# Performance work log

Hardware: AMD Instinct MI355X
Metric: run time of the kernel (lower is better)

The kernel has to match this reference:

```python
import jax, jax.numpy as jnp
import numpy as np

B, N_ELEC, N_NUC, D_EMB, D_MSG = 512, 32, 8, 128, 128


def idx_perm(n):
    # ordered pairs (i, j), i != j, shaped [n, n-1]
    i = np.repeat(np.arange(n), n - 1).reshape(n, n - 1)
    j = np.array([[k for k in range(n) if k != ii] for ii in range(n)])
    return jnp.asarray(i), jnp.asarray(j)


def pairwise_diffs(a, b):
    # a: [..., n, 3], b: [..., m, 3] -> [..., n, m, 4] (dx, dy, dz, |d|^2)
    d = a[..., :, None, :] - b[..., None, :, :]
    return jnp.concatenate([d, jnp.sum(d * d, axis=-1, keepdims=True)], axis=-1)


def mlp(x, w1, b1, w2, b2):
    return jax.nn.silu(x @ w1 + b1) @ w2 + b2


def setup_inputs() -> dict:
    key = jax.random.key(0)
    ks = jax.random.split(key, 10)
    sc = 0.1
    return {
        'rs': jax.random.normal(ks[0], (B, N_ELEC, 3), jnp.float32),
        'coords': jax.random.normal(ks[1], (N_NUC, 3), jnp.float32),
        'messages_el': jax.random.normal(ks[2], (B, N_ELEC, N_ELEC - 1, D_MSG), jnp.float32),
        'messages_nuc': jax.random.normal(ks[3], (B, N_ELEC, N_NUC, D_MSG), jnp.float32),
        'emb': jax.random.normal(ks[4], (B, N_ELEC, D_EMB), jnp.float32),
        'w1_el': jax.random.normal(ks[5], (D_EMB + D_MSG, 256), jnp.float32) * sc,
        'b1_el': jnp.zeros((256,), jnp.float32),
        'w2_el': jax.random.normal(ks[6], (256, 1), jnp.float32) * sc,
        'b2_el': jnp.zeros((1,), jnp.float32),
        'w1_nuc': jax.random.normal(ks[7], (D_EMB + D_MSG, 256), jnp.float32) * sc,
        'b1_nuc': jnp.zeros((256,), jnp.float32),
        'w2_nuc': jax.random.normal(ks[8], (256, 1), jnp.float32) * sc,
        'b2_nuc': jnp.zeros((1,), jnp.float32),
        'nuc_charges': jnp.array([6.0, 1.0, 1.0, 1.0, 1.0, 1.0, 1.0, 1.0], jnp.float32),
    }


def reference(rs, coords, messages_el, messages_nuc, emb,
              w1_el, b1_el, w2_el, b2_el,
              w1_nuc, b1_nuc, w2_nuc, b2_nuc, nuc_charges):
    n_elec, n_nuc = rs.shape[-2], coords.shape[0]
    emb_p = emb[:, :, None]  # [B, n_elec, 1, D_emb]
    # gather-concat features per pair
    f_el = jnp.concatenate(
        [jnp.broadcast_to(emb_p, (B, n_elec, n_elec - 1, D_EMB)), messages_el], axis=-1)
    f_nuc = jnp.concatenate(
        [jnp.broadcast_to(emb_p, (B, n_elec, n_nuc, D_EMB)), messages_nuc], axis=-1)
    i, j = idx_perm(n_elec)
    diffs_nuc = pairwise_diffs(rs, coords)  # [B, n_elec, n_nuc, 4]
    diffs_ee = pairwise_diffs(-rs, -rs)[:, i, j]  # [B, n_elec, n_elec-1, 4]
    diffs = jnp.concatenate([diffs_ee, diffs_nuc], axis=-2)
    f = jnp.concatenate(
        [mlp(f_el, w1_el, b1_el, w2_el, b2_el),
         mlp(f_nuc, w1_nuc, b1_nuc, w2_nuc, b2_nuc)], axis=-2)  # [B, n_elec, P, 1]
    ps = f * diffs[..., :3] / (1.0 + diffs[..., 3:] ** 1.5)
    ps = ps.sum(axis=-2)  # [B, n_elec, 3]
    # deeperwin decay
    decay = jnp.tanh(diffs_nuc[..., -1] / (0.5 / nuc_charges) ** 2).prod(axis=-1)
    return np.exp(-3.5).astype(np.float32) * decay[..., None] * ps
```

## Files before the change

kernel.cpp:

```cpp
#include <hip/hip_runtime.h>
#include <hip/hip_bf16.h>

#define OUT_SCALE 0.030197383422318501f

typedef __attribute__((ext_vector_type(8))) short bf16x8;
typedef __attribute__((ext_vector_type(4))) float f32x4;

#define EL_BLOCKS 1024
#define NUC_BLOCKS 1024

__device__ __forceinline__ unsigned pk2(float a, float b) {
  __hip_bfloat162 h = __float22bfloat162_rn(make_float2(a, b));
  unsigned u;
  __builtin_memcpy(&u, &h, 4);
  return u;
}

__device__ __forceinline__ float silu_f(float h) {
  return h * __builtin_amdgcn_rcpf(1.0f + __expf(-h));
}

__global__ void prep_w1(const float* __restrict__ w1a,
                        const float* __restrict__ w1b,
                        unsigned short* __restrict__ wp) {
  int gid = blockIdx.x * 256 + threadIdx.x;
  const float* w1 = (gid < 8192) ? w1a : w1b;
  int rem = gid & 8191;
  int kk = rem >> 10;
  int kg = (rem >> 8) & 3;
  int col = rem & 255;
  const float* src = w1 + (kk * 32 + kg * 8) * 256 + col;
  uint4 v;
  v.x = pk2(src[0 * 256], src[1 * 256]);
  v.y = pk2(src[2 * 256], src[3 * 256]);
  v.z = pk2(src[4 * 256], src[5 * 256]);
  v.w = pk2(src[6 * 256], src[7 * 256]);
  *(uint4*)(wp + (size_t)gid * 8) = v;
}

__global__ __launch_bounds__(512, 4) void bf_main_kernel(
    const float* __restrict__ rs, const float* __restrict__ msg_el,
    const float* __restrict__ msg_nuc, const float* __restrict__ emb,
    const unsigned short* __restrict__ wpk,
    const float* __restrict__ b1_el, const float* __restrict__ w2_el,
    const float* __restrict__ b2_el,
    const float* __restrict__ b1_nuc, const float* __restrict__ w2_nuc,
    const float* __restrict__ b2_nuc,
    const float* __restrict__ coords, const float* __restrict__ chg,
    float* __restrict__ out) {
  __shared__ __align__(16) unsigned short s_emb[16 * 128];
  __shared__ __align__(16) unsigned short s_msg[2 * 64 * 128];
  __shared__ __align__(16) float s_embc[16 * 256];
  __shared__ float s_fp[8][512];
  __shared__ float s_ps[16][4];
  __shared__ float s_decay[16];

  const int tid = threadIdx.x;
  const int bid = blockIdx.x;
  const int lane = tid & 63;
  const int wv = tid >> 6;
  const int cIdx = lane & 15, kg = lane >> 4;

  if (bid < EL_BLOCKS) {
    const int gp0 = bid * 16;
    const float* msg = msg_el;

    if (tid < 64) ((float*)s_ps)[tid] = 0.0f;

    if (tid < 256) {
      int p = tid >> 4, ch = tid & 15;
      const float* src = emb + (gp0 + p) * 128 + ch * 8;
      float4 v0 = *(const float4*)src;
      float4 v1 = *(const float4*)(src + 4);
      uint4 pk;
      pk.x = pk2(v0.x, v0.y); pk.y = pk2(v0.z, v0.w);
      pk.z = pk2(v1.x, v1.y); pk.w = pk2(v1.z, v1.w);
      *(uint4*)(s_emb + p * 128 + (ch ^ p) * 8) = pk;
    }

    bf16x8 Bf[4][2];
    float b1v[2][4], w2v[2][4];
    const int col = wv * 32 + cIdx;
#pragma unroll
    for (int nt = 0; nt < 2; ++nt) {
#pragma unroll
      for (int reg = 0; reg < 4; ++reg) {
        int h = wv * 32 + nt * 16 + kg * 4 + reg;
        b1v[nt][reg] = b1_el[h];
        w2v[nt][reg] = w2_el[h];
      }
#pragma unroll
      for (int kk = 0; kk < 4; ++kk)
        Bf[kk][nt] = *(const bf16x8*)(
            wpk + (size_t)((kk * 4 + kg) * 256 + col + nt * 16) * 8);
    }

    float4 la[2], lb[2];
#pragma unroll
    for (int u = 0; u < 2; ++u) {
      int id = u * 512 + tid;
      int lrw = id >> 4, ch = id & 15;
      int p = lrw >> 5, j = lrw & 31;
      int jc = j < 31 ? j : 30;
      const float* s = msg + (size_t)((gp0 + p) * 31 + jc) * 128 + ch * 8;
      la[u] = *(const float4*)s;
      lb[u] = *(const float4*)(s + 4);
    }

    __syncthreads();

    {
      f32x4 aE0 = {b1v[0][0], b1v[0][1], b1v[0][2], b1v[0][3]};
      f32x4 aE1 = {b1v[1][0], b1v[1][1], b1v[1][2], b1v[1][3]};
#pragma unroll
      for (int kk = 0; kk < 4; ++kk) {
        bf16x8 a = *(const bf16x8*)(
            s_emb + cIdx * 128 + ((kk * 4 + kg) ^ cIdx) * 8);
        aE0 = __builtin_amdgcn_mfma_f32_16x16x32_bf16(Bf[kk][0], a, aE0, 0, 0, 0);
        aE1 = __builtin_amdgcn_mfma_f32_16x16x32_bf16(Bf[kk][1], a, aE1, 0, 0, 0);
      }
      *(f32x4*)(s_embc + cIdx * 256 + wv * 32 + kg * 4) = aE0;
      *(f32x4*)(s_embc + cIdx * 256 + wv * 32 + 16 + kg * 4) = aE1;
    }

#pragma unroll
    for (int nt = 0; nt < 2; ++nt)
#pragma unroll
      for (int kk = 0; kk < 4; ++kk)
        Bf[kk][nt] = *(const bf16x8*)(
            wpk + (size_t)(((kk + 4) * 4 + kg) * 256 + col + nt * 16) * 8);

#pragma unroll
    for (int u = 0; u < 2; ++u) {
      int id = u * 512 + tid;
      int lrw = id >> 4, ch = id & 15;
      uint4 pk;
      pk.x = pk2(la[u].x, la[u].y); pk.y = pk2(la[u].z, la[u].w);
      pk.z = pk2(lb[u].x, lb[u].y); pk.w = pk2(lb[u].z, lb[u].w);
      *(uint4*)(s_msg + lrw * 128 + ((ch ^ (lrw & 15)) * 8)) = pk;
    }

    __syncthreads();

#pragma unroll 1
    for (int c = 0; c < 8; ++c) {
      if (c < 7) {
#pragma unroll
        for (int u = 0; u < 2; ++u) {
          int id = u * 512 + tid;
          int lrw = id >> 4, ch = id & 15;
          int p = ((c + 1) << 1) + (lrw >> 5);
          int j = lrw & 31;
          int jc = j < 31 ? j : 30;
          const float* s = msg + (size_t)((gp0 + p) * 31 + jc) * 128 + ch * 8;
          la[u] = *(const float4*)s;
          lb[u] = *(const float4*)(s + 4);
        }
      }
      const unsigned short* mb = s_msg + (c & 1) * 8192;
#pragma unroll
      for (int tt = 0; tt < 4; ++tt) {
        int p = (c << 1) + (tt >> 1);
        const float* ec = s_embc + p * 256;
        f32x4 acc0 = *(const f32x4*)(ec + wv * 32 + kg * 4);
        f32x4 acc1 = *(const f32x4*)(ec + wv * 32 + 16 + kg * 4);
        const unsigned short* mp = mb + (tt * 16 + cIdx) * 128;
#pragma unroll
        for (int kk = 0; kk < 4; ++kk) {
          bf16x8 a = *(const bf16x8*)(mp + ((kk * 4 + kg) ^ cIdx) * 8);
          acc0 = __builtin_amdgcn_mfma_f32_16x16x32_bf16(Bf[kk][0], a, acc0, 0, 0, 0);
          acc1 = __builtin_amdgcn_mfma_f32_16x16x32_bf16(Bf[kk][1], a, acc1, 0, 0, 0);
        }
        float p0 = 0.0f, p1 = 0.0f;
#pragma unroll
        for (int reg = 0; reg < 4; ++reg) {
          p0 += silu_f(acc0[reg]) * w2v[0][reg];
          p1 += silu_f(acc1[reg]) * w2v[1][reg];
        }
        float v = p0 + p1;
        v += __shfl_xor(v, 16);
        v += __shfl_xor(v, 32);
        if (kg == 0) s_fp[wv][c * 64 + tt * 16 + cIdx] = v;
      }
      if (c < 7) {
#pragma unroll
        for (int u = 0; u < 2; ++u) {
          int id = u * 512 + tid;
          int lrw = id >> 4, ch = id & 15;
          uint4 pk;
          pk.x = pk2(la[u].x, la[u].y); pk.y = pk2(la[u].z, la[u].w);
          pk.z = pk2(lb[u].x, lb[u].y); pk.w = pk2(lb[u].z, lb[u].w);
          *(uint4*)(s_msg + ((c + 1) & 1) * 8192 + lrw * 128 +
                    ((ch ^ (lrw & 15)) * 8)) = pk;
        }
      }
      __syncthreads();
    }

    if (tid < 496) {
      int p = tid / 31, jj = tid - p * 31;
      int gp = gp0 + p, b = gp >> 5, i = gp & 31;
      int jidx = jj + (jj >= i ? 1 : 0);
      const float* rsb = rs + b * 96;
      float dx = rsb[jidx * 3 + 0] - rsb[i * 3 + 0];
      float dy = rsb[jidx * 3 + 1] - rsb[i * 3 + 1];
      float dz = rsb[jidx * 3 + 2] - rsb[i * 3 + 2];
      float tq = dx * dx + dy * dy + dz * dz;
      int row = p * 32 + jj;
      float f = b2_el[0];
#pragma unroll
      for (int w = 0; w < 8; ++w) f += s_fp[w][row];
      float g = f * __builtin_amdgcn_rcpf(1.0f + tq * sqrtf(tq));
      atomicAdd(&s_ps[p][0], g * dx);
      atomicAdd(&s_ps[p][1], g * dy);
      atomicAdd(&s_ps[p][2], g * dz);
    }
    if (tid < 16) {
      int gp = gp0 + tid, b = gp >> 5, i = gp & 31;
      float x = rs[(b * 32 + i) * 3 + 0];
      float y = rs[(b * 32 + i) * 3 + 1];
      float z = rs[(b * 32 + i) * 3 + 2];
      float dcy = 1.0f;
#pragma unroll
      for (int n = 0; n < 8; ++n) {
        float dx = x - coords[n * 3 + 0];
        float dy = y - coords[n * 3 + 1];
        float dz = z - coords[n * 3 + 2];
        float tq = dx * dx + dy * dy + dz * dz;
        float zc = chg[n];
        dcy *= tanhf(4.0f * tq * zc * zc);
      }
      s_decay[tid] = dcy;
    }
    __syncthreads();
    if (tid < 48) {
      int p = tid / 3, c = tid - p * 3;
      int gp = gp0 + p;
      atomicAdd(&out[gp * 3 + c], OUT_SCALE * s_decay[p] * s_ps[p][c]);
    }
  } else {
    const int nbid = bid - EL_BLOCKS;
    const int gp0 = nbid * 16;
    const float* msg = msg_nuc;
    const unsigned short* wp = wpk + 8192 * 8;

    if (tid < 64) ((float*)s_ps)[tid] = 0.0f;

    if (tid < 256) {
      int p = tid >> 4, ch = tid & 15;
      const float* src = emb + (gp0 + p) * 128 + ch * 8;
      float4 v0 = *(const float4*)src;
      float4 v1 = *(const float4*)(src + 4);
      uint4 pk;
      pk.x = pk2(v0.x, v0.y); pk.y = pk2(v0.z, v0.w);
      pk.z = pk2(v1.x, v1.y); pk.w = pk2(v1.z, v1.w);
      *(uint4*)(s_emb + p * 128 + (ch ^ p) * 8) = pk;
    }

    bf16x8 Bf[4][2];
    float b1v[2][4], w2v[2][4];
    const int col = wv * 32 + cIdx;
#pragma unroll
    for (int nt = 0; nt < 2; ++nt) {
#pragma unroll
      for (int reg = 0; reg < 4; ++reg) {
        int h = wv * 32 + nt * 16 + kg * 4 + reg;
        b1v[nt][reg] = b1_nuc[h];
        w2v[nt][reg] = w2_nuc[h];
      }
#pragma unroll
      for (int kk = 0; kk < 4; ++kk)
        Bf[kk][nt] = *(const bf16x8*)(
            wp + (size_t)((kk * 4 + kg) * 256 + col + nt * 16) * 8);
    }

    float4 la[2], lb[2];
#pragma unroll
    for (int u = 0; u < 2; ++u) {
      int id = u * 512 + tid;
      int lrw = id >> 4, ch = id & 15;
      const float* s = msg + (size_t)(gp0 * 8 + lrw) * 128 + ch * 8;
      la[u] = *(const float4*)s;
      lb[u] = *(const float4*)(s + 4);
    }

    __syncthreads();

    {
      f32x4 aE0 = {b1v[0][0], b1v[0][1], b1v[0][2], b1v[0][3]};
      f32x4 aE1 = {b1v[1][0], b1v[1][1], b1v[1][2], b1v[1][3]};
#pragma unroll
      for (int kk = 0; kk < 4; ++kk) {
        bf16x8 a = *(const bf16x8*)(
            s_emb + cIdx * 128 + ((kk * 4 + kg) ^ cIdx) * 8);
        aE0 = __builtin_amdgcn_mfma_f32_16x16x32_bf16(Bf[kk][0], a, aE0, 0, 0, 0);
        aE1 = __builtin_amdgcn_mfma_f32_16x16x32_bf16(Bf[kk][1], a, aE1, 0, 0, 0);
      }
      *(f32x4*)(s_embc + cIdx * 256 + wv * 32 + kg * 4) = aE0;
      *(f32x4*)(s_embc + cIdx * 256 + wv * 32 + 16 + kg * 4) = aE1;
    }

#pragma unroll
    for (int nt = 0; nt < 2; ++nt)
#pragma unroll
      for (int kk = 0; kk < 4; ++kk)
        Bf[kk][nt] = *(const bf16x8*)(
            wp + (size_t)(((kk + 4) * 4 + kg) * 256 + col + nt * 16) * 8);

#pragma unroll
    for (int u = 0; u < 2; ++u) {
      int id = u * 512 + tid;
      int lrw = id >> 4, ch = id & 15;
      uint4 pk;
      pk.x = pk2(la[u].x, la[u].y); pk.y = pk2(la[u].z, la[u].w);
      pk.z = pk2(lb[u].x, lb[u].y); pk.w = pk2(lb[u].z, lb[u].w);
      *(uint4*)(s_msg + lrw * 128 + ((ch ^ (lrw & 15)) * 8)) = pk;
    }

    __syncthreads();

#pragma unroll 1
    for (int c = 0; c < 2; ++c) {
      if (c < 1) {
#pragma unroll
        for (int u = 0; u < 2; ++u) {
          int id = u * 512 + tid;
          int lrw = id >> 4, ch = id & 15;
          const float* s = msg + (size_t)(gp0 * 8 + 64 + lrw) * 128 + ch * 8;
          la[u] = *(const float4*)s;
          lb[u] = *(const float4*)(s + 4);
        }
      }
      const unsigned short* mb = s_msg + (c & 1) * 8192;
#pragma unroll
      for (int tt = 0; tt < 4; ++tt) {
        int t = c * 4 + tt;
        int r = t * 16 + cIdx;
        int p = r >> 3;
        const float* ec = s_embc + p * 256;
        f32x4 acc0 = *(const f32x4*)(ec + wv * 32 + kg * 4);
        f32x4 acc1 = *(const f32x4*)(ec + wv * 32 + 16 + kg * 4);
        const unsigned short* mp = mb + (r & 63) * 128;
#pragma unroll
        for (int kk = 0; kk < 4; ++kk) {
          bf16x8 a = *(const bf16x8*)(mp + ((kk * 4 + kg) ^ cIdx) * 8);
          acc0 = __builtin_amdgcn_mfma_f32_16x16x32_bf16(Bf[kk][0], a, acc0, 0, 0, 0);
          acc1 = __builtin_amdgcn_mfma_f32_16x16x32_bf16(Bf[kk][1], a, acc1, 0, 0, 0);
        }
        float p0 = 0.0f, p1 = 0.0f;
#pragma unroll
        for (int reg = 0; reg < 4; ++reg) {
          p0 += silu_f(acc0[reg]) * w2v[0][reg];
          p1 += silu_f(acc1[reg]) * w2v[1][reg];
        }
        float v = p0 + p1;
        v += __shfl_xor(v, 16);
        v += __shfl_xor(v, 32);
        if (kg == 0) s_fp[wv][t * 16 + cIdx] = v;
      }
      if (c < 1) {
#pragma unroll
        for (int u = 0; u < 2; ++u) {
          int id = u * 512 + tid;
          int lrw = id >> 4, ch = id & 15;
          uint4 pk;
          pk.x = pk2(la[u].x, la[u].y); pk.y = pk2(la[u].z, la[u].w);
          pk.z = pk2(lb[u].x, lb[u].y); pk.w = pk2(lb[u].z, lb[u].w);
          *(uint4*)(s_msg + 8192 + lrw * 128 + ((ch ^ (lrw & 15)) * 8)) = pk;
        }
      }
      __syncthreads();
    }

    if (tid < 128) {
      int p = tid >> 3, n = tid & 7;
      int gp = gp0 + p, b = gp >> 5, i = gp & 31;
      float dx = rs[(b * 32 + i) * 3 + 0] - coords[n * 3 + 0];
      float dy = rs[(b * 32 + i) * 3 + 1] - coords[n * 3 + 1];
      float dz = rs[(b * 32 + i) * 3 + 2] - coords[n * 3 + 2];
      float tq = dx * dx + dy * dy + dz * dz;
      float f = b2_nuc[0];
#pragma unroll
      for (int w = 0; w < 8; ++w) f += s_fp[w][tid];
      float g = f * __builtin_amdgcn_rcpf(1.0f + tq * sqrtf(tq));
      atomicAdd(&s_ps[p][0], g * dx);
      atomicAdd(&s_ps[p][1], g * dy);
      atomicAdd(&s_ps[p][2], g * dz);
    }
    if (tid < 16) {
      int gp = gp0 + tid, b = gp >> 5, i = gp & 31;
      float x = rs[(b * 32 + i) * 3 + 0];
      float y = rs[(b * 32 + i) * 3 + 1];
      float z = rs[(b * 32 + i) * 3 + 2];
      float dcy = 1.0f;
#pragma unroll
      for (int n = 0; n < 8; ++n) {
        float dx = x - coords[n * 3 + 0];
        float dy = y - coords[n * 3 + 1];
        float dz = z - coords[n * 3 + 2];
        float tq = dx * dx + dy * dy + dz * dz;
        float zc = chg[n];
        dcy *= tanhf(4.0f * tq * zc * zc);
      }
      s_decay[tid] = dcy;
    }
    __syncthreads();
    if (tid < 48) {
      int p = tid / 3, c = tid - p * 3;
      int gp = gp0 + p;
      atomicAdd(&out[gp * 3 + c], OUT_SCALE * s_decay[p] * s_ps[p][c]);
    }
  }
}

extern "C" void kernel_launch(void* const* d_in, const int* in_sizes, int n_in,
                              void* d_out, int out_size, void* d_ws, size_t ws_size,
                              hipStream_t stream) {
  const float* rs       = (const float*)d_in[0];
  const float* coords   = (const float*)d_in[1];
  const float* msg_el   = (const float*)d_in[2];
  const float* msg_nuc  = (const float*)d_in[3];
  const float* emb      = (const float*)d_in[4];
  const float* w1_el    = (const float*)d_in[5];
  const float* b1_el    = (const float*)d_in[6];
  const float* w2_el    = (const float*)d_in[7];
  const float* b2_el    = (const float*)d_in[8];
  const float* w1_nuc   = (const float*)d_in[9];
  const float* b1_nuc   = (const float*)d_in[10];
  const float* w2_nuc   = (const float*)d_in[11];
  const float* b2_nuc   = (const float*)d_in[12];
  const float* chg      = (const float*)d_in[13];
  float* out = (float*)d_out;

  unsigned short* wpk = (unsigned short*)d_ws;

  hipMemsetAsync(out, 0, (size_t)out_size * sizeof(float), stream);
  prep_w1<<<64, 256, 0, stream>>>(w1_el, w1_nuc, wpk);
  bf_main_kernel<<<EL_BLOCKS + NUC_BLOCKS, 512, 0, stream>>>(
      rs, msg_el, msg_nuc, emb, wpk, b1_el, w2_el, b2_el, b1_nuc, w2_nuc,
      b2_nuc, coords, chg, out);
}
```

Measured before the change: 114.8 us.

## Merge electron and nucleus blocks so each block handles both MLPs and writes output directly

Each block now runs the electron-pair MLP and then the nucleus-pair MLP for the same 16 electrons, instead of splitting them across separate blocks. This halves the grid, computes decay and output once per electron, and replaces global atomics plus the output memset with plain stores. The cost is a longer serial chain per block, less parallelism across blocks, and a slightly larger shared-memory footprint.

```diff
diff --git a/kernel.cpp b/kernel.cpp
--- a/kernel.cpp
+++ b/kernel.cpp
@@ -6,8 +6,7 @@
 typedef __attribute__((ext_vector_type(8))) short bf16x8;
 typedef __attribute__((ext_vector_type(4))) float f32x4;
 
-#define EL_BLOCKS 1024
-#define NUC_BLOCKS 1024
+#define NBLOCKS 1024
 
 __device__ __forceinline__ unsigned pk2(float a, float b) {
   __hip_bfloat162 h = __float22bfloat162_rn(make_float2(a, b));
@@ -51,7 +50,8 @@
   __shared__ __align__(16) unsigned short s_emb[16 * 128];
   __shared__ __align__(16) unsigned short s_msg[2 * 64 * 128];
   __shared__ __align__(16) float s_embc[16 * 256];
-  __shared__ float s_fp[8][512];
+  __shared__ float s_fpe[8][512];
+  __shared__ float s_fpn[8][128];
   __shared__ float s_ps[16][4];
   __shared__ float s_decay[16];
 
@@ -60,356 +60,305 @@
   const int lane = tid & 63;
   const int wv = tid >> 6;
   const int cIdx = lane & 15, kg = lane >> 4;
-
-  if (bid < EL_BLOCKS) {
-    const int gp0 = bid * 16;
-    const float* msg = msg_el;
-
-    if (tid < 64) ((float*)s_ps)[tid] = 0.0f;
-
-    if (tid < 256) {
-      int p = tid >> 4, ch = tid & 15;
-      const float* src = emb + (gp0 + p) * 128 + ch * 8;
-      float4 v0 = *(const float4*)src;
-      float4 v1 = *(const float4*)(src + 4);
-      uint4 pk;
-      pk.x = pk2(v0.x, v0.y); pk.y = pk2(v0.z, v0.w);
-      pk.z = pk2(v1.x, v1.y); pk.w = pk2(v1.z, v1.w);
-      *(uint4*)(s_emb + p * 128 + (ch ^ p) * 8) = pk;
-    }
-
-    bf16x8 Bf[4][2];
-    float b1v[2][4], w2v[2][4];
-    const int col = wv * 32 + cIdx;
-#pragma unroll
-    for (int nt = 0; nt < 2; ++nt) {
+  const int gp0 = bid * 16;
+  const int col = wv * 32 + cIdx;
+
+  if (tid < 64) ((float*)s_ps)[tid] = 0.0f;
+
+  if (tid < 256) {
+    int p = tid >> 4, ch = tid & 15;
+    const float* src = emb + (gp0 + p) * 128 + ch * 8;
+    float4 v0 = *(const float4*)src;
+    float4 v1 = *(const float4*)(src + 4);
+    uint4 pk;
+    pk.x = pk2(v0.x, v0.y); pk.y = pk2(v0.z, v0.w);
+    pk.z = pk2(v1.x, v1.y); pk.w = pk2(v1.z, v1.w);
+    *(uint4*)(s_emb + p * 128 + (ch ^ p) * 8) = pk;
+  }
+
+  bf16x8 Bf[4][2];
+  float b1v[2][4], w2v[2][4];
+#pragma unroll
+  for (int nt = 0; nt < 2; ++nt) {
+#pragma unroll
+    for (int reg = 0; reg < 4; ++reg) {
+      int h = wv * 32 + nt * 16 + kg * 4 + reg;
+      b1v[nt][reg] = b1_el[h];
+      w2v[nt][reg] = w2_el[h];
+    }
+#pragma unroll
+    for (int kk = 0; kk < 4; ++kk)
+      Bf[kk][nt] = *(const bf16x8*)(
+          wpk + (size_t)((kk * 4 + kg) * 256 + col + nt * 16) * 8);
+  }
+
+  float4 la[2], lb[2];
+#pragma unroll
+  for (int u = 0; u < 2; ++u) {
+    int id = u * 512 + tid;
+    int lrw = id >> 4, ch = id & 15;
+    int p = lrw >> 5, j = lrw & 31;
+    int jc = j < 31 ? j : 30;
+    const float* s = msg_el + (size_t)((gp0 + p) * 31 + jc) * 128 + ch * 8;
+    la[u] = *(const float4*)s;
+    lb[u] = *(const float4*)(s + 4);
+  }
+
+  __syncthreads();
+
+  {
+    f32x4 aE0 = {b1v[0][0], b1v[0][1], b1v[0][2], b1v[0][3]};
+    f32x4 aE1 = {b1v[1][0], b1v[1][1], b1v[1][2], b1v[1][3]};
+#pragma unroll
+    for (int kk = 0; kk < 4; ++kk) {
+      bf16x8 a = *(const bf16x8*)(
+          s_emb + cIdx * 128 + ((kk * 4 + kg) ^ cIdx) * 8);
+      aE0 = __builtin_amdgcn_mfma_f32_16x16x32_bf16(Bf[kk][0], a, aE0, 0, 0, 0);
+      aE1 = __builtin_amdgcn_mfma_f32_16x16x32_bf16(Bf[kk][1], a, aE1, 0, 0, 0);
+    }
+    *(f32x4*)(s_embc + cIdx * 256 + wv * 32 + kg * 4) = aE0;
+    *(f32x4*)(s_embc + cIdx * 256 + wv * 32 + 16 + kg * 4) = aE1;
+  }
+
+#pragma unroll
+  for (int nt = 0; nt < 2; ++nt)
+#pragma unroll
+    for (int kk = 0; kk < 4; ++kk)
+      Bf[kk][nt] = *(const bf16x8*)(
+          wpk + (size_t)(((kk + 4) * 4 + kg) * 256 + col + nt * 16) * 8);
+
+#pragma unroll
+  for (int u = 0; u < 2; ++u) {
+    int id = u * 512 + tid;
+    int lrw = id >> 4, ch = id & 15;
+    uint4 pk;
+    pk.x = pk2(la[u].x, la[u].y); pk.y = pk2(la[u].z, la[u].w);
+    pk.z = pk2(lb[u].x, lb[u].y); pk.w = pk2(lb[u].z, lb[u].w);
+    *(uint4*)(s_msg + lrw * 128 + ((ch ^ (lrw & 15)) * 8)) = pk;
+  }
+
+  __syncthreads();
+
+#pragma unroll 1
+  for (int c = 0; c < 8; ++c) {
+    if (c < 7) {
+#pragma unroll
+      for (int u = 0; u < 2; ++u) {
+        int id = u * 512 + tid;
+        int lrw = id >> 4, ch = id & 15;
+        int p = ((c + 1) << 1) + (lrw >> 5);
+        int j = lrw & 31;
+        int jc = j < 31 ? j : 30;
+        const float* s = msg_el + (size_t)((gp0 + p) * 31 + jc) * 128 + ch * 8;
+        la[u] = *(const float4*)s;
+        lb[u] = *(const float4*)(s + 4);
+      }
+    }
+    const unsigned short* mb = s_msg + (c & 1) * 8192;
+#pragma unroll
+    for (int tt = 0; tt < 4; ++tt) {
+      int p = (c << 1) + (tt >> 1);
+      const float* ec = s_embc + p * 256;
+      f32x4 acc0 = *(const f32x4*)(ec + wv * 32 + kg * 4);
+      f32x4 acc1 = *(const f32x4*)(ec + wv * 32 + 16 + kg * 4);
+      const unsigned short* mp = mb + (tt * 16 + cIdx) * 128;
+#pragma unroll
+      for (int kk = 0; kk < 4; ++kk) {
+        bf16x8 a = *(const bf16x8*)(mp + ((kk * 4 + kg) ^ cIdx) * 8);
+        acc0 = __builtin_amdgcn_mfma_f32_16x16x32_bf16(Bf[kk][0], a, acc0, 0, 0, 0);
+        acc1 = __builtin_amdgcn_mfma_f32_16x16x32_bf16(Bf[kk][1], a, acc1, 0, 0, 0);
+      }
+      float p0 = 0.0f, p1 = 0.0f;
 #pragma unroll
       for (int reg = 0; reg < 4; ++reg) {
-        int h = wv * 32 + nt * 16 + kg * 4 + reg;
-        b1v[nt][reg] = b1_el[h];
-        w2v[nt][reg] = w2_el[h];
-      }
-#pragma unroll
-      for (int kk = 0; kk < 4; ++kk)
-        Bf[kk][nt] = *(const bf16x8*)(
-            wpk + (size_t)((kk * 4 + kg) * 256 + col + nt * 16) * 8);
-    }
-
-    float4 la[2], lb[2];
-#pragma unroll
-    for (int u = 0; u < 2; ++u) {
-      int id = u * 512 + tid;
-      int lrw = id >> 4, ch = id & 15;
-      int p = lrw >> 5, j = lrw & 31;
-      int jc = j < 31 ? j : 30;
-      const float* s = msg + (size_t)((gp0 + p) * 31 + jc) * 128 + ch * 8;
-      la[u] = *(const float4*)s;
-      lb[u] = *(const float4*)(s + 4);
-    }
-
+        p0 += silu_f(acc0[reg]) * w2v[0][reg];
+        p1 += silu_f(acc1[reg]) * w2v[1][reg];
+      }
+      float v = p0 + p1;
+      v += __shfl_xor(v, 16);
+      v += __shfl_xor(v, 32);
+      if (kg == 0) s_fpe[wv][c * 64 + tt * 16 + cIdx] = v;
+    }
+    if (c < 7) {
+#pragma unroll
+      for (int u = 0; u < 2; ++u) {
+        int id = u * 512 + tid;
+        int lrw = id >> 4, ch = id & 15;
+        uint4 pk;
+        pk.x = pk2(la[u].x, la[u].y); pk.y = pk2(la[u].z, la[u].w);
+        pk.z = pk2(lb[u].x, lb[u].y); pk.w = pk2(lb[u].z, lb[u].w);
+        *(uint4*)(s_msg + ((c + 1) & 1) * 8192 + lrw * 128 +
+                  ((ch ^ (lrw & 15)) * 8)) = pk;
+      }
+    }
     __syncthreads();
-
-    {
-      f32x4 aE0 = {b1v[0][0], b1v[0][1], b1v[0][2], b1v[0][3]};
-      f32x4 aE1 = {b1v[1][0], b1v[1][1], b1v[1][2], b1v[1][3]};
+  }
+
+  const unsigned short* wpn = wpk + 8192 * 8;
+#pragma unroll
+  for (int nt = 0; nt < 2; ++nt) {
+#pragma unroll
+    for (int reg = 0; reg < 4; ++reg) {
+      int h = wv * 32 + nt * 16 + kg * 4 + reg;
+      b1v[nt][reg] = b1_nuc[h];
+      w2v[nt][reg] = w2_nuc[h];
+    }
+#pragma unroll
+    for (int kk = 0; kk < 4; ++kk)
+      Bf[kk][nt] = *(const bf16x8*)(
+          wpn + (size_t)((kk * 4 + kg) * 256 + col + nt * 16) * 8);
+  }
+
+#pragma unroll
+  for (int u = 0; u < 2; ++u) {
+    int id = u * 512 + tid;
+    int lrw = id >> 4, ch = id & 15;
+    const float* s = msg_nuc + (size_t)(gp0 * 8 + lrw) * 128 + ch * 8;
+    la[u] = *(const float4*)s;
+    lb[u] = *(const float4*)(s + 4);
+  }
+
+  {
+    f32x4 aE0 = {b1v[0][0], b1v[0][1], b1v[0][2], b1v[0][3]};
+    f32x4 aE1 = {b1v[1][0], b1v[1][1], b1v[1][2], b1v[1][3]};
+#pragma unroll
+    for (int kk = 0; kk < 4; ++kk) {
+      bf16x8 a = *(const bf16x8*)(
+          s_emb + cIdx * 128 + ((kk * 4 + kg) ^ cIdx) * 8);
+      aE0 = __builtin_amdgcn_mfma_f32_16x16x32_bf16(Bf[kk][0], a, aE0, 0, 0, 0);
+      aE1 = __builtin_amdgcn_mfma_f32_16x16x32_bf16(Bf[kk][1], a, aE1, 0, 0, 0);
+    }
+    *(f32x4*)(s_embc + cIdx * 256 + wv * 32 + kg * 4) = aE0;
+    *(f32x4*)(s_embc + cIdx * 256 + wv * 32 + 16 + kg * 4) = aE1;
+  }
+
+#pragma unroll
+  for (int nt = 0; nt < 2; ++nt)
+#pragma unroll
+    for (int kk = 0; kk < 4; ++kk)
+      Bf[kk][nt] = *(const bf16x8*)(
+          wpn + (size_t)(((kk + 4) * 4 + kg) * 256 + col + nt * 16) * 8);
+
+#pragma unroll
+  for (int u = 0; u < 2; ++u) {
+    int id = u * 512 + tid;
+    int lrw = id >> 4, ch = id & 15;
+    uint4 pk;
+    pk.x = pk2(la[u].x, la[u].y); pk.y = pk2(la[u].z, la[u].w);
+    pk.z = pk2(lb[u].x, lb[u].y); pk.w = pk2(lb[u].z, lb[u].w);
+    *(uint4*)(s_msg + lrw * 128 + ((ch ^ (lrw & 15)) * 8)) = pk;
+  }
+
+  __syncthreads();
+
+#pragma unroll 1
+  for (int c = 0; c < 2; ++c) {
+    if (c < 1) {
+#pragma unroll
+      for (int u = 0; u < 2; ++u) {
+        int id = u * 512 + tid;
+        int lrw = id >> 4, ch = id & 15;
+        const float* s = msg_nuc + (size_t)(gp0 * 8 + 64 + lrw) * 128 + ch * 8;
+        la[u] = *(const float4*)s;
+        lb[u] = *(const float4*)(s + 4);
+      }
+    }
+    const unsigned short* mb = s_msg + (c & 1) * 8192;
+#pragma unroll
+    for (int tt = 0; tt < 4; ++tt) {
+      int t = c * 4 + tt;
+      int r = t * 16 + cIdx;
+      int p = r >> 3;
+      const float* ec = s_embc + p * 256;
+      f32x4 acc0 = *(const f32x4*)(ec + wv * 32 + kg * 4);
+      f32x4 acc1 = *(const f32x4*)(ec + wv * 32 + 16 + kg * 4);
+      const unsigned short* mp = mb + (r & 63) * 128;
 #pragma unroll
       for (int kk = 0; kk < 4; ++kk) {
-        bf16x8 a = *(const bf16x8*)(
-            s_emb + cIdx * 128 + ((kk * 4 + kg) ^ cIdx) * 8);
-        aE0 = __builtin_amdgcn_mfma_f32_16x16x32_bf16(Bf[kk][0], a, aE0, 0, 0, 0);
-        aE1 = __builtin_amdgcn_mfma_f32_16x16x32_bf16(Bf[kk][1], a, aE1, 0, 0, 0);
-      }
-      *(f32x4*)(s_embc + cIdx * 256 + wv * 32 + kg * 4) = aE0;
-      *(f32x4*)(s_embc + cIdx * 256 + wv * 32 + 16 + kg * 4) = aE1;
-    }
-
-#pragma unroll
-    for (int nt = 0; nt < 2; ++nt)
-#pragma unroll
-      for (int kk = 0; kk < 4; ++kk)
-        Bf[kk][nt] = *(const bf16x8*)(
-            wpk + (size_t)(((kk + 4) * 4 + kg) * 256 + col + nt * 16) * 8);
-
-#pragma unroll
-    for (int u = 0; u < 2; ++u) {
-      int id = u * 512 + tid;
-      int lrw = id >> 4, ch = id & 15;
-      uint4 pk;
-      pk.x = pk2(la[u].x, la[u].y); pk.y = pk2(la[u].z, la[u].w);
-      pk.z = pk2(lb[u].x, lb[u].y); pk.w = pk2(lb[u].z, lb[u].w);
-      *(uint4*)(s_msg + lrw * 128 + ((ch ^ (lrw & 15)) * 8)) = pk;
-    }
-
+        bf16x8 a = *(const bf16x8*)(mp + ((kk * 4 + kg) ^ cIdx) * 8);
+        acc0 = __builtin_amdgcn_mfma_f32_16x16x32_bf16(Bf[kk][0], a, acc0, 0, 0, 0);
+        acc1 = __builtin_amdgcn_mfma_f32_16x16x32_bf16(Bf[kk][1], a, acc1, 0, 0, 0);
+      }
+      float p0 = 0.0f, p1 = 0.0f;
+#pragma unroll
+      for (int reg = 0; reg < 4; ++reg) {
+        p0 += silu_f(acc0[reg]) * w2v[0][reg];
+        p1 += silu_f(acc1[reg]) * w2v[1][reg];
+      }
+      float v = p0 + p1;
+      v += __shfl_xor(v, 16);
+      v += __shfl_xor(v, 32);
+      if (kg == 0) s_fpn[wv][t * 16 + cIdx] = v;
+    }
+    if (c < 1) {
+#pragma unroll
+      for (int u = 0; u < 2; ++u) {
+        int id = u * 512 + tid;
+        int lrw = id >> 4, ch = id & 15;
+        uint4 pk;
+        pk.x = pk2(la[u].x, la[u].y); pk.y = pk2(la[u].z, la[u].w);
+        pk.z = pk2(lb[u].x, lb[u].y); pk.w = pk2(lb[u].z, lb[u].w);
+        *(uint4*)(s_msg + 8192 + lrw * 128 + ((ch ^ (lrw & 15)) * 8)) = pk;
+      }
+    }
     __syncthreads();
-
-#pragma unroll 1
-    for (int c = 0; c < 8; ++c) {
-      if (c < 7) {
-#pragma unroll
-        for (int u = 0; u < 2; ++u) {
-          int id = u * 512 + tid;
-          int lrw = id >> 4, ch = id & 15;
-          int p = ((c + 1) << 1) + (lrw >> 5);
-          int j = lrw & 31;
-          int jc = j < 31 ? j : 30;
-          const float* s = msg + (size_t)((gp0 + p) * 31 + jc) * 128 + ch * 8;
-          la[u] = *(const float4*)s;
-          lb[u] = *(const float4*)(s + 4);
-        }
-      }
-      const unsigned short* mb = s_msg + (c & 1) * 8192;
-#pragma unroll
-      for (int tt = 0; tt < 4; ++tt) {
-        int p = (c << 1) + (tt >> 1);
-        const float* ec = s_embc + p * 256;
-        f32x4 acc0 = *(const f32x4*)(ec + wv * 32 + kg * 4);
-        f32x4 acc1 = *(const f32x4*)(ec + wv * 32 + 16 + kg * 4);
-        const unsigned short* mp = mb + (tt * 16 + cIdx) * 128;
-#pragma unroll
-        for (int kk = 0; kk < 4; ++kk) {
-          bf16x8 a = *(const bf16x8*)(mp + ((kk * 4 + kg) ^ cIdx) * 8);
-          acc0 = __builtin_amdgcn_mfma_f32_16x16x32_bf16(Bf[kk][0], a, acc0, 0, 0, 0);
-          acc1 = __builtin_amdgcn_mfma_f32_16x16x32_bf16(Bf[kk][1], a, acc1, 0, 0, 0);
-        }
-        float p0 = 0.0f, p1 = 0.0f;
-#pragma unroll
-        for (int reg = 0; reg < 4; ++reg) {
-          p0 += silu_f(acc0[reg]) * w2v[0][reg];
-          p1 += silu_f(acc1[reg]) * w2v[1][reg];
-        }
-        float v = p0 + p1;
-        v += __shfl_xor(v, 16);
-        v += __shfl_xor(v, 32);
-        if (kg == 0) s_fp[wv][c * 64 + tt * 16 + cIdx] = v;
-      }
-      if (c < 7) {
-#pragma unroll
-        for (int u = 0; u < 2; ++u) {
-          int id = u * 512 + tid;
-          int lrw = id >> 4, ch = id & 15;
-          uint4 pk;
-          pk.x = pk2(la[u].x, la[u].y); pk.y = pk2(la[u].z, la[u].w);
-          pk.z = pk2(lb[u].x, lb[u].y); pk.w = pk2(lb[u].z, lb[u].w);
-          *(uint4*)(s_msg + ((c + 1) & 1) * 8192 + lrw * 128 +
-                    ((ch ^ (lrw & 15)) * 8)) = pk;
-        }
-      }
-      __syncthreads();
-    }
-
-    if (tid < 496) {
-      int p = tid / 31, jj = tid - p * 31;
-      int gp = gp0 + p, b = gp >> 5, i = gp & 31;
-      int jidx = jj + (jj >= i ? 1 : 0);
-      const float* rsb = rs + b * 96;
-      float dx = rsb[jidx * 3 + 0] - rsb[i * 3 + 0];
-      float dy = rsb[jidx * 3 + 1] - rsb[i * 3 + 1];
-      float dz = rsb[jidx * 3 + 2] - rsb[i * 3 + 2];
+  }
+
+  if (tid < 496) {
+    int p = tid / 31, jj = tid - p * 31;
+    int gp = gp0 + p, b = gp >> 5, i = gp & 31;
+    int jidx = jj + (jj >= i ? 1 : 0);
+    const float* rsb = rs + b * 96;
+    float dx = rsb[jidx * 3 + 0] - rsb[i * 3 + 0];
+    float dy = rsb[jidx * 3 + 1] - rsb[i * 3 + 1];
+    float dz = rsb[jidx * 3 + 2] - rsb[i * 3 + 2];
+    float tq = dx * dx + dy * dy + dz * dz;
+    int row = p * 32 + jj;
+    float f = b2_el[0];
+#pragma unroll
+    for (int w = 0; w < 8; ++w) f += s_fpe[w][row];
+    float g = f * __builtin_amdgcn_rcpf(1.0f + tq * sqrtf(tq));
+    atomicAdd(&s_ps[p][0], g * dx);
+    atomicAdd(&s_ps[p][1], g * dy);
+    atomicAdd(&s_ps[p][2], g * dz);
+  }
+  if (tid < 128) {
+    int p = tid >> 3, n = tid & 7;
+    int gp = gp0 + p, b = gp >> 5, i = gp & 31;
+    float dx = rs[(b * 32 + i) * 3 + 0] - coords[n * 3 + 0];
+    float dy = rs[(b * 32 + i) * 3 + 1] - coords[n * 3 + 1];
+    float dz = rs[(b * 32 + i) * 3 + 2] - coords[n * 3 + 2];
+    float tq = dx * dx + dy * dy + dz * dz;
+    float f = b2_nuc[0];
+#pragma unroll
+    for (int w = 0; w < 8; ++w) f += s_fpn[w][tid];
+    float g = f * __builtin_amdgcn_rcpf(1.0f + tq * sqrtf(tq));
+    atomicAdd(&s_ps[p][0], g * dx);
+    atomicAdd(&s_ps[p][1], g * dy);
+    atomicAdd(&s_ps[p][2], g * dz);
+  }
+  if (tid < 16) {
+    int gp = gp0 + tid, b = gp >> 5, i = gp & 31;
+    float x = rs[(b * 32 + i) * 3 + 0];
+    float y = rs[(b * 32 + i) * 3 + 1];
+    float z = rs[(b * 32 + i) * 3 + 2];
+    float dcy = 1.0f;
+#pragma unroll
+    for (int n = 0; n < 8; ++n) {
+      float dx = x - coords[n * 3 + 0];
+      float dy = y - coords[n * 3 + 1];
+      float dz = z - coords[n * 3 + 2];
       float tq = dx * dx + dy * dy + dz * dz;
-      int row = p * 32 + jj;
-      float f = b2_el[0];
-#pragma unroll
-      for (int w = 0; w < 8; ++w) f += s_fp[w][row];
-      float g = f * __builtin_amdgcn_rcpf(1.0f + tq * sqrtf(tq));
-      atomicAdd(&s_ps[p][0], g * dx);
-      atomicAdd(&s_ps[p][1], g * dy);
-      atomicAdd(&s_ps[p][2], g * dz);
-    }
-    if (tid < 16) {
-      int gp = gp0 + tid, b = gp >> 5, i = gp & 31;
-      float x = rs[(b * 32 + i) * 3 + 0];
-      float y = rs[(b * 32 + i) * 3 + 1];
-      float z = rs[(b * 32 + i) * 3 + 2];
-      float dcy = 1.0f;
-#pragma unroll
-      for (int n = 0; n < 8; ++n) {
-        float dx = x - coords[n * 3 + 0];
-        float dy = y - coords[n * 3 + 1];
-        float dz = z - coords[n * 3 + 2];
-        float tq = dx * dx + dy * dy + dz * dz;
-        float zc = chg[n];
-        dcy *= tanhf(4.0f * tq * zc * zc);
-      }
-      s_decay[tid] = dcy;
-    }
-    __syncthreads();
-    if (tid < 48) {
-      int p = tid / 3, c = tid - p * 3;
-      int gp = gp0 + p;
-      atomicAdd(&out[gp * 3 + c], OUT_SCALE * s_decay[p] * s_ps[p][c]);
-    }
-  } else {
-    const int nbid = bid - EL_BLOCKS;
-    const int gp0 = nbid * 16;
-    const float* msg = msg_nuc;
-    const unsigned short* wp = wpk + 8192 * 8;
-
-    if (tid < 64) ((float*)s_ps)[tid] = 0.0f;
-
-    if (tid < 256) {
-      int p = tid >> 4, ch = tid & 15;
-      const float* src = emb + (gp0 + p) * 128 + ch * 8;
-      float4 v0 = *(const float4*)src;
-      float4 v1 = *(const float4*)(src + 4);
-      uint4 pk;
-      pk.x = pk2(v0.x, v0.y); pk.y = pk2(v0.z, v0.w);
-      pk.z = pk2(v1.x, v1.y); pk.w = pk2(v1.z, v1.w);
-      *(uint4*)(s_emb + p * 128 + (ch ^ p) * 8) = pk;
-    }
-
-    bf16x8 Bf[4][2];
-    float b1v[2][4], w2v[2][4];
-    const int col = wv * 32 + cIdx;
-#pragma unroll
-    for (int nt = 0; nt < 2; ++nt) {
-#pragma unroll
-      for (int reg = 0; reg < 4; ++reg) {
-        int h = wv * 32 + nt * 16 + kg * 4 + reg;
-        b1v[nt][reg] = b1_nuc[h];
-        w2v[nt][reg] = w2_nuc[h];
-      }
-#pragma unroll
-      for (int kk = 0; kk < 4; ++kk)
-        Bf[kk][nt] = *(const bf16x8*)(
-            wp + (size_t)((kk * 4 + kg) * 256 + col + nt * 16) * 8);
-    }
-
-    float4 la[2], lb[2];
-#pragma unroll
-    for (int u = 0; u < 2; ++u) {
-      int id = u * 512 + tid;
-      int lrw = id >> 4, ch = id & 15;
-      const float* s = msg + (size_t)(gp0 * 8 + lrw) * 128 + ch * 8;
-      la[u] = *(const float4*)s;
-      lb[u] = *(const float4*)(s + 4);
-    }
-
-    __syncthreads();
-
-    {
-      f32x4 aE0 = {b1v[0][0], b1v[0][1], b1v[0][2], b1v[0][3]};
-      f32x4 aE1 = {b1v[1][0], b1v[1][1], b1v[1][2], b1v[1][3]};
-#pragma unroll
-      for (int kk = 0; kk < 4; ++kk) {
-        bf16x8 a = *(const bf16x8*)(
-            s_emb + cIdx * 128 + ((kk * 4 + kg) ^ cIdx) * 8);
-        aE0 = __builtin_amdgcn_mfma_f32_16x16x32_bf16(Bf[kk][0], a, aE0, 0, 0, 0);
-        aE1 = __builtin_amdgcn_mfma_f32_16x16x32_bf16(Bf[kk][1], a, aE1, 0, 0, 0);
-      }
-      *(f32x4*)(s_embc + cIdx * 256 + wv * 32 + kg * 4) = aE0;
-      *(f32x4*)(s_embc + cIdx * 256 + wv * 32 + 16 + kg * 4) = aE1;
-    }
-
-#pragma unroll
-    for (int nt = 0; nt < 2; ++nt)
-#pragma unroll
-      for (int kk = 0; kk < 4; ++kk)
-        Bf[kk][nt] = *(const bf16x8*)(
-            wp + (size_t)(((kk + 4) * 4 + kg) * 256 + col + nt * 16) * 8);
-
-#pragma unroll
-    for (int u = 0; u < 2; ++u) {
-      int id = u * 512 + tid;
-      int lrw = id >> 4, ch = id & 15;
-      uint4 pk;
-      pk.x = pk2(la[u].x, la[u].y); pk.y = pk2(la[u].z, la[u].w);
-      pk.z = pk2(lb[u].x, lb[u].y); pk.w = pk2(lb[u].z, lb[u].w);
-      *(uint4*)(s_msg + lrw * 128 + ((ch ^ (lrw & 15)) * 8)) = pk;
-    }
-
-    __syncthreads();
-
-#pragma unroll 1
-    for (int c = 0; c < 2; ++c) {
-      if (c < 1) {
-#pragma unroll
-        for (int u = 0; u < 2; ++u) {
-          int id = u * 512 + tid;
-          int lrw = id >> 4, ch = id & 15;
-          const float* s = msg + (size_t)(gp0 * 8 + 64 + lrw) * 128 + ch * 8;
-          la[u] = *(const float4*)s;
-          lb[u] = *(const float4*)(s + 4);
-        }
-      }
-      const unsigned short* mb = s_msg + (c & 1) * 8192;
-#pragma unroll
-      for (int tt = 0; tt < 4; ++tt) {
-        int t = c * 4 + tt;
-        int r = t * 16 + cIdx;
-        int p = r >> 3;
-        const float* ec = s_embc + p * 256;
-        f32x4 acc0 = *(const f32x4*)(ec + wv * 32 + kg * 4);
-        f32x4 acc1 = *(const f32x4*)(ec + wv * 32 + 16 + kg * 4);
-        const unsigned short* mp = mb + (r & 63) * 128;
-#pragma unroll
-        for (int kk = 0; kk < 4; ++kk) {
-          bf16x8 a = *(const bf16x8*)(mp + ((kk * 4 + kg) ^ cIdx) * 8);
-          acc0 = __builtin_amdgcn_mfma_f32_16x16x32_bf16(Bf[kk][0], a, acc0, 0, 0, 0);
-          acc1 = __builtin_amdgcn_mfma_f32_16x16x32_bf16(Bf[kk][1], a, acc1, 0, 0, 0);
-        }
-        float p0 = 0.0f, p1 = 0.0f;
-#pragma unroll
-        for (int reg = 0; reg < 4; ++reg) {
-          p0 += silu_f(acc0[reg]) * w2v[0][reg];
-          p1 += silu_f(acc1[reg]) * w2v[1][reg];
-        }
-        float v = p0 + p1;
-        v += __shfl_xor(v, 16);
-        v += __shfl_xor(v, 32);
-        if (kg == 0) s_fp[wv][t * 16 + cIdx] = v;
-      }
-      if (c < 1) {
-#pragma unroll
-        for (int u = 0; u < 2; ++u) {
-          int id = u * 512 + tid;
-          int lrw = id >> 4, ch = id & 15;
-          uint4 pk;
-          pk.x = pk2(la[u].x, la[u].y); pk.y = pk2(la[u].z, la[u].w);
-          pk.z = pk2(lb[u].x, lb[u].y); pk.w = pk2(lb[u].z, lb[u].w);
-          *(uint4*)(s_msg + 8192 + lrw * 128 + ((ch ^ (lrw & 15)) * 8)) = pk;
-        }
-      }
-      __syncthreads();
-    }
-
-    if (tid < 128) {
-      int p = tid >> 3, n = tid & 7;
-      int gp = gp0 + p, b = gp >> 5, i = gp & 31;
-      float dx = rs[(b * 32 + i) * 3 + 0] - coords[n * 3 + 0];
-      float dy = rs[(b * 32 + i) * 3 + 1] - coords[n * 3 + 1];
-      float dz = rs[(b * 32 + i) * 3 + 2] - coords[n * 3 + 2];
-      float tq = dx * dx + dy * dy + dz * dz;
-      float f = b2_nuc[0];
-#pragma unroll
-      for (int w = 0; w < 8; ++w) f += s_fp[w][tid];
-      float g = f * __builtin_amdgcn_rcpf(1.0f + tq * sqrtf(tq));
-      atomicAdd(&s_ps[p][0], g * dx);
-      atomicAdd(&s_ps[p][1], g * dy);
-      atomicAdd(&s_ps[p][2], g * dz);
-    }
-    if (tid < 16) {
-      int gp = gp0 + tid, b = gp >> 5, i = gp & 31;
-      float x = rs[(b * 32 + i) * 3 + 0];
-      float y = rs[(b * 32 + i) * 3 + 1];
-      float z = rs[(b * 32 + i) * 3 + 2];
-      float dcy = 1.0f;
-#pragma unroll
-      for (int n = 0; n < 8; ++n) {
-        float dx = x - coords[n * 3 + 0];
-        float dy = y - coords[n * 3 + 1];
-        float dz = z - coords[n * 3 + 2];
-        float tq = dx * dx + dy * dy + dz * dz;
-        float zc = chg[n];
-        dcy *= tanhf(4.0f * tq * zc * zc);
-      }
-      s_decay[tid] = dcy;
-    }
-    __syncthreads();
-    if (tid < 48) {
-      int p = tid / 3, c = tid - p * 3;
-      int gp = gp0 + p;
-      atomicAdd(&out[gp * 3 + c], OUT_SCALE * s_decay[p] * s_ps[p][c]);
-    }
+      float zc = chg[n];
+      dcy *= tanhf(4.0f * tq * zc * zc);
+    }
+    s_decay[tid] = dcy;
+  }
+  __syncthreads();
+  if (tid < 48) {
+    int p = tid / 3, c = tid - p * 3;
+    int gp = gp0 + p;
+    out[gp * 3 + c] = OUT_SCALE * s_decay[p] * s_ps[p][c];
   }
 }
 
@@ -434,9 +383,8 @@
 
   unsigned short* wpk = (unsigned short*)d_ws;
 
-  hipMemsetAsync(out, 0, (size_t)out_size * sizeof(float), stream);
   prep_w1<<<64, 256, 0, stream>>>(w1_el, w1_nuc, wpk);
-  bf_main_kernel<<<EL_BLOCKS + NUC_BLOCKS, 512, 0, stream>>>(
+  bf_main_kernel<<<NBLOCKS, 512, 0, stream>>>(
       rs, msg_el, msg_nuc, emb, wpk, b1_el, w2_el, b2_el, b1_nuc, w2_nuc,
       b2_nuc, coords, chg, out);
 }
```

New measurement: 126.5 us. +10.1%, slower.
